# Kernel optimization log

Hardware: AMD Instinct MI355X
Metric: run time of the kernel (lower is better)

Reference implementation:

```python
import jax, jax.numpy as jnp
import numpy as np

H = 16        # num_attention_heads
KVH = 4       # num_key_value_heads
D = 128       # head_dim
K = 5         # query multiplier k
HID = 2048    # hidden_size = H * D
THETA = 10000.0


def rotate_half(x):
    h = x.shape[-1] // 2
    return jnp.concatenate([-x[..., h:], x[..., :h]], axis=-1)


def setup_inputs() -> dict:
    key = jax.random.key(0)
    ks = jax.random.split(key, 6)
    B, S = 1, 1024
    q_len = S - 1
    hidden_states = jax.random.normal(ks[0], (B, S, HID), jnp.float32)
    prev_hidden_states = jax.random.normal(ks[1], (B, S - 1, HID), jnp.float32)
    causal = jnp.tril(jnp.ones((q_len, q_len), bool))
    attention_mask = jnp.where(causal, 0.0, -1e9).astype(jnp.float32)[None, None]  # (1,1,q,kv)
    position_ids = jnp.arange(q_len, dtype=jnp.int64)[None]  # (1, kv_len)
    Wq = jax.random.normal(ks[2], (HID, H * D * K), jnp.float32) * 0.02
    Wkv = jax.random.normal(ks[3], (2 * HID, 2 * KVH * D), jnp.float32) * 0.02
    Wo = jax.random.normal(ks[4], (HID, HID), jnp.float32) * 0.02
    return {
        'hidden_states': hidden_states,
        'prev_hidden_states': prev_hidden_states,
        'attention_mask': attention_mask,
        'position_ids': position_ids,
        'Wq': Wq,
        'Wkv': Wkv,
        'Wo': Wo,
    }


def reference(hidden_states, prev_hidden_states, attention_mask, position_ids, Wq, Wkv, Wo):
    B = hidden_states.shape[0]  # must be 1 for this module's broadcasting
    # feature-dim concat of previous layer states with shifted current states
    prev = jnp.concatenate([prev_hidden_states, hidden_states[:, :-1]], axis=-1)  # (B, S-1, 2*HID)
    hs = hidden_states[:, 1:]  # training-mode slice -> (B, q_len, HID)
    q_len = hs.shape[1]
    kv_len = prev.shape[1]

    q = hs @ Wq                       # (B, q_len, H*D*K)
    kv = prev @ Wkv                   # (B, kv_len, 2*KVH*D)
    k_st, v_st = jnp.split(kv, 2, axis=-1)

    # faithful raw reshape: (B, q_len, H*D*K) -> (B*K, q_len, H, D) -> (B*K, H, q_len, D)
    q = q.reshape(B * K, -1, H, D).transpose(0, 2, 1, 3)
    k_st = k_st.reshape(B, kv_len, KVH, D).transpose(0, 2, 1, 3)   # (B, KVH, kv, D)
    v_st = v_st.reshape(B, kv_len, KVH, D).transpose(0, 2, 1, 3)

    # RoPE (LlamaRotaryEmbedding)
    inv_freq = 1.0 / (THETA ** (jnp.arange(0, D, 2, dtype=jnp.float32) / D))  # (D/2,)
    freqs = position_ids.astype(jnp.float32)[..., None] * inv_freq            # (B, kv, D/2)
    emb = jnp.concatenate([freqs, freqs], axis=-1)                            # (B, kv, D)
    cos = jnp.cos(emb)[:, None]  # (B, 1, kv, D)
    sin = jnp.sin(emb)[:, None]
    q = q * cos[..., -q_len:, :] + rotate_half(q) * sin[..., -q_len:, :]
    k_st = k_st * cos[..., :kv_len, :] + rotate_half(k_st) * sin[..., :kv_len, :]

    # repeat_kv: (B, KVH, kv, D) -> (B, H, kv, D)
    n_rep = H // KVH
    k_rep = jnp.repeat(k_st, n_rep, axis=1)
    v_rep = jnp.repeat(v_st, n_rep, axis=1)

    # (B*K, H, q, D) @ (B, H, D, kv) -> broadcast over k variants (B==1)
    attn = jnp.matmul(q, jnp.swapaxes(k_rep, -1, -2)) / jnp.sqrt(jnp.float32(D))
    attn = attn + attention_mask
    attn = jax.nn.softmax(attn.astype(jnp.float32), axis=-1).astype(q.dtype)
    out = jnp.matmul(attn, v_rep)                 # (B*K, H, q, D)
    out = out.transpose(0, 2, 1, 3).reshape(B * K, q_len, HID)
    return out @ Wo                                # (B*K, q_len, HID)
```

## Files before the change

kernel.cpp:

```cpp
#include <hip/hip_runtime.h>
#include <cstddef>
#include <cstdint>

#define SQ    1023
#define HIDC  2048
#define NQC   10240
#define NKVC  1024

typedef unsigned short ushort_t;
typedef __bf16 bf16x8 __attribute__((ext_vector_type(8)));
typedef float  f32x4  __attribute__((ext_vector_type(4)));

__device__ __forceinline__ ushort_t f2bf(float x) {
  union { float f; uint32_t u; } v; v.f = x;
  uint32_t r = v.u + 0x7fffu + ((v.u >> 16) & 1u);
  return (ushort_t)(r >> 16);
}

__device__ __forceinline__ ushort_t f2bf_fast(float x) {
  __bf16 b = (__bf16)x;
  return __builtin_bit_cast(ushort_t, b);
}

__global__ void k_tables(float* __restrict__ cosT, float* __restrict__ sinT) {
  int idx = blockIdx.x * blockDim.x + threadIdx.x;
  if (idx >= SQ * 64) return;
  int t = idx >> 6, i = idx & 63;
  float inv = powf(10000.0f, -(float)i * (1.0f / 64.0f));
  float f = (float)t * inv;
  cosT[idx] = cosf(f);
  sinT[idx] = sinf(f);
}

__global__ void k_rope_q(const float* __restrict__ q, ushort_t* __restrict__ qb,
                         const float* __restrict__ cosT, const float* __restrict__ sinT) {
  int idx = blockIdx.x * blockDim.x + threadIdx.x;
  if (idx >= 5115 * 16 * 64) return;
  int d  = idx & 63;
  int h  = (idx >> 6) & 15;
  int st = idx >> 10;
  int t  = st % 1023;
  size_t base = (((size_t)st * 16) + h) * 128 + d;
  float x0 = q[base], x1 = q[base + 64];
  float c = cosT[t * 64 + d], s = sinT[t * 64 + d];
  const float sc = 0.1275174485f;
  qb[base]      = f2bf((x0 * c - x1 * s) * sc);
  qb[base + 64] = f2bf((x1 * c + x0 * s) * sc);
}

__global__ void k_rope_k(const float* __restrict__ kvp, ushort_t* __restrict__ kb,
                         const float* __restrict__ cosT, const float* __restrict__ sinT) {
  int idx = blockIdx.x * blockDim.x + threadIdx.x;
  if (idx >= SQ * 4 * 64) return;
  int d   = idx & 63;
  int kvh = (idx >> 6) & 3;
  int t   = idx >> 8;
  size_t src = (size_t)t * 1024 + kvh * 128 + d;
  float x0 = 0.f, x1 = 0.f;
  #pragma unroll
  for (int z = 0; z < 4; ++z) {
    x0 += kvp[(size_t)z * (SQ * 1024) + src];
    x1 += kvp[(size_t)z * (SQ * 1024) + src + 64];
  }
  float c = cosT[t * 64 + d], s = sinT[t * 64 + d];
  size_t dst = (size_t)t * 512 + kvh * 128 + d;
  kb[dst]      = f2bf(x0 * c - x1 * s);
  kb[dst + 64] = f2bf(x1 * c + x0 * s);
}

__global__ __launch_bounds__(256)
void k_vtrans(const float* __restrict__ kvp, ushort_t* __restrict__ vt) {
  __shared__ float tile[32][33];
  int v0 = blockIdx.x * 32;
  int t0 = blockIdx.y * 32;
  int r = threadIdx.x >> 5, c = threadIdx.x & 31;
  #pragma unroll
  for (int p = 0; p < 4; ++p) {
    int t = t0 + p * 8 + r;
    float s = 0.f;
    if (t < SQ) {
      size_t src = (size_t)t * 1024 + 512 + v0 + c;
      #pragma unroll
      for (int z = 0; z < 4; ++z) s += kvp[(size_t)z * (SQ * 1024) + src];
    }
    tile[p * 8 + r][c] = s;
  }
  __syncthreads();
  #pragma unroll
  for (int p = 0; p < 4; ++p) {
    int v = v0 + p * 8 + r;
    vt[(size_t)v * 1024 + t0 + c] = f2bf(tile[c][p * 8 + r]);
  }
}

__global__ void k_f2b(const float* __restrict__ in, ushort_t* __restrict__ out, int n) {
  int i = (blockIdx.x * blockDim.x + threadIdx.x) * 4;
  if (i >= n) return;
  float4 v = *reinterpret_cast<const float4*>(in + i);
  uint2 pk;
  pk.x = (uint32_t)f2bf(v.x) | ((uint32_t)f2bf(v.y) << 16);
  pk.y = (uint32_t)f2bf(v.z) | ((uint32_t)f2bf(v.w) << 16);
  *reinterpret_cast<uint2*>(out + i) = pk;
}

__global__ void k_concat_b(const float* __restrict__ prevh, const float* __restrict__ hidden,
                           ushort_t* __restrict__ out) {
  int i = (blockIdx.x * blockDim.x + threadIdx.x) * 4;
  if (i >= SQ * 4096) return;
  int r = i >> 12, c = i & 4095;
  const float* src = (c < 2048) ? (prevh + (size_t)r * 2048 + c)
                                : (hidden + (size_t)r * 2048 + (c - 2048));
  float4 v = *reinterpret_cast<const float4*>(src);
  uint2 pk;
  pk.x = (uint32_t)f2bf(v.x) | ((uint32_t)f2bf(v.y) << 16);
  pk.y = (uint32_t)f2bf(v.z) | ((uint32_t)f2bf(v.w) << 16);
  *reinterpret_cast<uint2*>(out + (size_t)r * 4096 + c) = pk;
}

__global__ __launch_bounds__(256)
void k_tconv(const float* __restrict__ in, ushort_t* __restrict__ out, int K, int N) {
  __shared__ float t[32][33];
  int n0 = blockIdx.x * 32, k0 = blockIdx.y * 32;
  int r = threadIdx.x >> 5, c = threadIdx.x & 31;
  #pragma unroll
  for (int p = 0; p < 4; ++p)
    t[p * 8 + r][c] = in[(size_t)(k0 + p * 8 + r) * N + n0 + c];
  __syncthreads();
  #pragma unroll
  for (int p = 0; p < 4; ++p)
    out[(size_t)(n0 + p * 8 + r) * K + k0 + c] = f2bf(t[c][p * 8 + r]);
}

__global__ __launch_bounds__(256)
void k_gemm3buf(const ushort_t* __restrict__ A, const ushort_t* __restrict__ Bt,
                float* __restrict__ C, int M, int N, int Kd)
{
  __shared__ __align__(16) ushort_t As[3][128 * 32];
  __shared__ __align__(16) ushort_t Bs[3][128 * 32];

  const int tid  = threadIdx.x;
  const int lane = tid & 63;
  const int w    = tid >> 6;
  const int wm   = w >> 1, wn = w & 1;
  const int fr   = lane & 15;
  const int kg   = (lane >> 4) * 8;
  const int m0   = blockIdx.y * 128, n0 = blockIdx.x * 128;

  const int lrow = lane >> 2;
  const int lk   = (lane & 3) * 8;

  f32x4 acc[4][4];
  #pragma unroll
  for (int i = 0; i < 4; ++i)
    #pragma unroll
    for (int j = 0; j < 4; ++j) acc[i][j] = (f32x4){0.f, 0.f, 0.f, 0.f};

  auto STAGE = [&](int b, int k0) {
    #pragma unroll
    for (int c = 0; c < 2; ++c) {
      int ch  = w + c * 4;
      int row = ch * 16 + lrow;
      const ushort_t* ga = A  + (size_t)(m0 + row) * Kd + k0 + lk;
      const ushort_t* gb = Bt + (size_t)(n0 + row) * Kd + k0 + lk;
      __builtin_amdgcn_global_load_lds(
          (const __attribute__((address_space(1))) void*)ga,
          (__attribute__((address_space(3))) void*)(&As[b][0] + ch * 512), 16, 0, 0);
      __builtin_amdgcn_global_load_lds(
          (const __attribute__((address_space(1))) void*)gb,
          (__attribute__((address_space(3))) void*)(&Bs[b][0] + ch * 512), 16, 0, 0);
    }
  };

  const int nt = Kd / 32;
  STAGE(0, 0);
  STAGE(1, 32);

  int cur = 0;
  for (int t = 0; t < nt; ++t) {
    if (t + 1 < nt) {
      asm volatile("s_waitcnt vmcnt(4)" ::: "memory");
    } else {
      asm volatile("s_waitcnt vmcnt(0)" ::: "memory");
    }
    __builtin_amdgcn_s_barrier();
    if (t + 2 < nt) {
      int sb = cur + 2; if (sb >= 3) sb -= 3;
      STAGE(sb, (t + 2) * 32);
    }

    bf16x8 av[4], bv[4];
    #pragma unroll
    for (int mi = 0; mi < 4; ++mi)
      av[mi] = *reinterpret_cast<const bf16x8*>(&As[cur][0] + (wm * 64 + mi * 16 + fr) * 32 + kg);
    #pragma unroll
    for (int nj = 0; nj < 4; ++nj)
      bv[nj] = *reinterpret_cast<const bf16x8*>(&Bs[cur][0] + (wn * 64 + nj * 16 + fr) * 32 + kg);
    #pragma unroll
    for (int mi = 0; mi < 4; ++mi)
      #pragma unroll
      for (int nj = 0; nj < 4; ++nj)
        acc[mi][nj] = __builtin_amdgcn_mfma_f32_16x16x32_bf16(av[mi], bv[nj], acc[mi][nj], 0, 0, 0);

    cur = (cur == 2) ? 0 : cur + 1;
  }

  #pragma unroll
  for (int mi = 0; mi < 4; ++mi) {
    #pragma unroll
    for (int nj = 0; nj < 4; ++nj) {
      int rbase = m0 + wm * 64 + mi * 16 + (lane >> 4) * 4;
      int col   = n0 + wn * 64 + nj * 16 + fr;
      #pragma unroll
      for (int r = 0; r < 4; ++r) {
        int gr = rbase + r;
        if (gr < M) C[(size_t)gr * N + col] = acc[mi][nj][r];
      }
    }
  }
}

__global__ __launch_bounds__(256)
void k_gemm64(const ushort_t* __restrict__ A, const ushort_t* __restrict__ Bt,
              float* __restrict__ C, int M, int N, int Kd, int kLen)
{
  __shared__ __align__(16) ushort_t As[64 * 32];
  __shared__ __align__(16) ushort_t Bs[128 * 32];

  const int tid  = threadIdx.x;
  const int lane = tid & 63;
  const int w    = tid >> 6;
  const int wm   = w >> 1, wn = w & 1;
  const int fr   = lane & 15;
  const int kg   = (lane >> 4) * 8;
  const int g4   = lane >> 4;
  const int l15  = lane & 15;
  const int m0   = blockIdx.y * 64, n0 = blockIdx.x * 128;
  const int kOff = blockIdx.z * kLen;
  C += (size_t)blockIdx.z * M * N;

  const int arow = tid >> 2, aslot = (tid & 3) * 8;

  f32x4 acc[2][4];
  #pragma unroll
  for (int i = 0; i < 2; ++i)
    #pragma unroll
    for (int j = 0; j < 4; ++j) acc[i][j] = (f32x4){0.f, 0.f, 0.f, 0.f};

  for (int k0 = kOff; k0 < kOff + kLen; k0 += 32) {
    {
      const ushort_t* ga = A + (size_t)(m0 + arow) * Kd + k0 + aslot;
      __builtin_amdgcn_global_load_lds(
          (const __attribute__((address_space(1))) void*)ga,
          (__attribute__((address_space(3))) void*)(As + w * 512), 16, 0, 0);
    }
    #pragma unroll
    for (int c = 0; c < 2; ++c) {
      int u = c * 256 + tid;
      const ushort_t* gb = Bt + (size_t)(n0 + (u >> 2)) * Kd + k0 + (u & 3) * 8;
      __builtin_amdgcn_global_load_lds(
          (const __attribute__((address_space(1))) void*)gb,
          (__attribute__((address_space(3))) void*)(Bs + (c * 256 + w * 64) * 8), 16, 0, 0);
    }
    __syncthreads();

    bf16x8 av[2], bv[4];
    #pragma unroll
    for (int mi = 0; mi < 2; ++mi)
      av[mi] = *reinterpret_cast<const bf16x8*>(As + (wm * 32 + mi * 16 + fr) * 32 + kg);
    #pragma unroll
    for (int nj = 0; nj < 4; ++nj)
      bv[nj] = *reinterpret_cast<const bf16x8*>(Bs + (wn * 64 + nj * 16 + fr) * 32 + kg);
    #pragma unroll
    for (int mi = 0; mi < 2; ++mi)
      #pragma unroll
      for (int nj = 0; nj < 4; ++nj)
        acc[mi][nj] = __builtin_amdgcn_mfma_f32_16x16x32_bf16(av[mi], bv[nj], acc[mi][nj], 0, 0, 0);
    __syncthreads();
  }

  #pragma unroll
  for (int mi = 0; mi < 2; ++mi) {
    #pragma unroll
    for (int nj = 0; nj < 4; ++nj) {
      int rbase = m0 + wm * 32 + mi * 16 + g4 * 4;
      int col   = n0 + wn * 64 + nj * 16 + l15;
      #pragma unroll
      for (int r = 0; r < 4; ++r) {
        int gr = rbase + r;
        if (gr < M) C[(size_t)gr * N + col] = acc[mi][nj][r];
      }
    }
  }
}

__global__ __launch_bounds__(256)
void k_attn_mfma(const ushort_t* __restrict__ qb, const ushort_t* __restrict__ kb,
                 const ushort_t* __restrict__ vt, ushort_t* __restrict__ oattb)
{
  __shared__ __align__(16) ushort_t Ks[64 * 128];
  __shared__ __align__(16) ushort_t Vs[128 * 64];
  __shared__ __align__(16) ushort_t Ps[4][16 * 64];

  const int tid  = threadIdx.x;
  const int lane = tid & 63;
  const int w    = tid >> 6;
  const int l15  = lane & 15;
  const int g4   = lane >> 4;
  const int gh   = blockIdx.x;
  const int g = gh >> 4, h = gh & 15, kvh = (gh & 15) >> 2;
  const int qt = 15 - blockIdx.y;
  const int t0 = qt * 64;

  bf16x8 av[4];
  {
    int t = t0 + w * 16 + l15;
    const ushort_t* qrow = qb + (((size_t)(g * SQ + t)) * 16 + h) * 128;
    #pragma unroll
    for (int kk = 0; kk < 4; ++kk)
      av[kk] = *reinterpret_cast<const bf16x8*>(qrow + kk * 32 + g4 * 8);
  }

  f32x4 acc[8];
  #pragma unroll
  for (int dt = 0; dt < 8; ++dt) acc[dt] = (f32x4){0.f, 0.f, 0.f, 0.f};
  float m[4], l[4];
  #pragma unroll
  for (int r = 0; r < 4; ++r) { m[r] = -1e30f; l[r] = 0.f; }

  ushort_t* pw = &Ps[w][0];

  for (int jt = 0; jt <= qt; ++jt) {
    int u0 = jt * 64;
    #pragma unroll
    for (int i = 0; i < 4; ++i) {
      int c = (w * 4 + i) * 64 + lane;
      int kv = c >> 4, sl = c & 15;
      const ushort_t* srck = kb + (size_t)(u0 + kv) * 512 + kvh * 128 + ((sl ^ (kv & 7)) << 3);
      __builtin_amdgcn_global_load_lds(
          (const __attribute__((address_space(1))) void*)srck,
          (__attribute__((address_space(3))) void*)(Ks + (w * 4 + i) * 512), 16, 0, 0);
      int d = c >> 3, sv = c & 7;
      const ushort_t* srcv = vt + (size_t)(kvh * 128 + d) * 1024 + u0 + ((sv ^ (d & 7)) << 3);
      __builtin_amdgcn_global_load_lds(
          (const __attribute__((address_space(1))) void*)srcv,
          (__attribute__((address_space(3))) void*)(Vs + (w * 4 + i) * 512), 16, 0, 0);
    }
    __syncthreads();

    f32x4 S[4];
    #pragma unroll
    for (int ct = 0; ct < 4; ++ct) S[ct] = (f32x4){0.f, 0.f, 0.f, 0.f};
    #pragma unroll
    for (int ct = 0; ct < 4; ++ct) {
      int kv = ct * 16 + l15;
      #pragma unroll
      for (int kk = 0; kk < 4; ++kk) {
        bf16x8 bv = *reinterpret_cast<const bf16x8*>(
            Ks + kv * 128 + ((((kk << 2) | g4) ^ (kv & 7)) << 3));
        S[ct] = __builtin_amdgcn_mfma_f32_16x16x32_bf16(av[kk], bv, S[ct], 0, 0, 0);
      }
    }
    if (jt == qt) {
      #pragma unroll
      for (int ct = 0; ct < 4; ++ct) {
        int u = u0 + ct * 16 + l15;
        #pragma unroll
        for (int r = 0; r < 4; ++r) {
          int t = t0 + w * 16 + g4 * 4 + r;
          if (u > t) S[ct][r] = -1e30f;
        }
      }
    }
    float tm[4];
    #pragma unroll
    for (int r = 0; r < 4; ++r) {
      float t1 = fmaxf(fmaxf(S[0][r], S[1][r]), fmaxf(S[2][r], S[3][r]));
      t1 = fmaxf(t1, __shfl_xor(t1, 1));
      t1 = fmaxf(t1, __shfl_xor(t1, 2));
      t1 = fmaxf(t1, __shfl_xor(t1, 4));
      t1 = fmaxf(t1, __shfl_xor(t1, 8));
      tm[r] = t1;
    }
    bool need = (tm[0] > m[0] + 8.f) || (tm[1] > m[1] + 8.f) ||
                (tm[2] > m[2] + 8.f) || (tm[3] > m[3] + 8.f);
    if (__any(need)) {
      #pragma unroll
      for (int r = 0; r < 4; ++r) {
        float mn = fmaxf(m[r], tm[r]);
        float corr = exp2f(m[r] - mn);
        m[r] = mn;
        l[r] *= corr;
        #pragma unroll
        for (int dt = 0; dt < 8; ++dt) acc[dt][r] *= corr;
      }
    }
    #pragma unroll
    for (int r = 0; r < 4; ++r) {
      float ps = 0.f;
      #pragma unroll
      for (int ct = 0; ct < 4; ++ct) {
        float p = exp2f(S[ct][r] - m[r]);
        S[ct][r] = p;
        ps += p;
      }
      ps += __shfl_xor(ps, 1);
      ps += __shfl_xor(ps, 2);
      ps += __shfl_xor(ps, 4);
      ps += __shfl_xor(ps, 8);
      l[r] += ps;
    }

    #pragma unroll
    for (int ct = 0; ct < 4; ++ct) {
      int kv = ct * 16 + l15;
      #pragma unroll
      for (int r = 0; r < 4; ++r) {
        int q = g4 * 4 + r;
        pw[q * 64 + ((((kv >> 3) ^ (q & 7)) << 3) | (kv & 7))] = f2bf_fast(S[ct][r]);
      }
    }
    #pragma unroll
    for (int kk = 0; kk < 2; ++kk) {
      bf16x8 pa = *reinterpret_cast<const bf16x8*>(
          pw + l15 * 64 + ((((kk << 2) | g4) ^ (l15 & 7)) << 3));
      #pragma unroll
      for (int dt = 0; dt < 8; ++dt) {
        int d = dt * 16 + l15;
        bf16x8 vv = *reinterpret_cast<const bf16x8*>(
            Vs + d * 64 + ((((kk << 2) | g4) ^ (d & 7)) << 3));
        acc[dt] = __builtin_amdgcn_mfma_f32_16x16x32_bf16(pa, vv, acc[dt], 0, 0, 0);
      }
    }
    __syncthreads();
  }

  #pragma unroll
  for (int r = 0; r < 4; ++r) {
    int t = t0 + w * 16 + g4 * 4 + r;
    if (t >= SQ) continue;
    float inv = 1.f / l[r];
    ushort_t* dst = oattb + ((size_t)(g * SQ + t)) * 2048 + h * 128;
    #pragma unroll
    for (int dt = 0; dt < 8; ++dt)
      dst[dt * 16 + l15] = f2bf_fast(acc[dt][r] * inv);
  }
}

extern "C" void kernel_launch(void* const* d_in, const int* in_sizes, int n_in,
                              void* d_out, int out_size, void* d_ws, size_t ws_size,
                              hipStream_t stream) {
  const float* hidden = (const float*)d_in[0];
  const float* prevh  = (const float*)d_in[1];
  const float* Wq     = (const float*)d_in[4];
  const float* Wkv    = (const float*)d_in[5];
  const float* Wo     = (const float*)d_in[6];
  float* out = (float*)d_out;

  char* ws = (char*)d_ws;
  float*    kvp   = (float*)ws;                        ws += (size_t)4 * SQ * 1024 * 4;
  float*    cosT  = (float*)ws;                        ws += (size_t)65472 * 4;
  float*    sinT  = (float*)ws;                        ws += (size_t)65472 * 4;
  ushort_t* qbb   = (ushort_t*)ws;                     ws += (size_t)5120 * 2048 * 2;
  ushort_t* kb    = (ushort_t*)ws;                     ws += (size_t)1024 * 512 * 2;
  ushort_t* vtb   = (ushort_t*)ws;                     ws += (size_t)512 * 1024 * 2;
  ushort_t* hbf   = (ushort_t*)ws;                     ws += (size_t)1024 * 2048 * 2;
  ushort_t* akv   = (ushort_t*)ws;                     ws += (size_t)1024 * 4096 * 2;
  ushort_t* oattb = (ushort_t*)ws;                     ws += (size_t)5120 * 2048 * 2;
  ushort_t* wqt   = (ushort_t*)ws;                     ws += (size_t)10240 * 2048 * 2;
  ushort_t* wkvt  = (ushort_t*)ws;                     ws += (size_t)1024 * 4096 * 2;
  ushort_t* wot   = (ushort_t*)ws;                     ws += (size_t)2048 * 2048 * 2;

  float* qp = out;

  k_tables<<<dim3((SQ * 64 + 255) / 256), dim3(256), 0, stream>>>(cosT, sinT);

  k_tconv<<<dim3(NQC / 32, HIDC / 32), dim3(256), 0, stream>>>(Wq, wqt, HIDC, NQC);
  k_tconv<<<dim3(NKVC / 32, 4096 / 32), dim3(256), 0, stream>>>(Wkv, wkvt, 4096, NKVC);
  k_tconv<<<dim3(HIDC / 32, HIDC / 32), dim3(256), 0, stream>>>(Wo, wot, HIDC, HIDC);

  k_f2b<<<dim3((SQ * 2048 / 4 + 255) / 256), dim3(256), 0, stream>>>(hidden + 2048, hbf, SQ * 2048);
  k_concat_b<<<dim3((SQ * 4096 / 4 + 255) / 256), dim3(256), 0, stream>>>(prevh, hidden, akv);

  k_gemm3buf<<<dim3(NQC / 128, 8), dim3(256), 0, stream>>>(hbf, wqt, qp, SQ, NQC, 2048);
  k_gemm64<<<dim3(NKVC / 128, 16, 4), dim3(256), 0, stream>>>(akv, wkvt, kvp, SQ, NKVC, 4096, 1024);

  k_rope_q<<<dim3((5115 * 16 * 64 + 255) / 256), dim3(256), 0, stream>>>(qp, qbb, cosT, sinT);
  k_rope_k<<<dim3((SQ * 4 * 64 + 255) / 256), dim3(256), 0, stream>>>(kvp, kb, cosT, sinT);
  k_vtrans<<<dim3(16, 32), dim3(256), 0, stream>>>(kvp, vtb);

  k_attn_mfma<<<dim3(80, 16), dim3(256), 0, stream>>>(qbb, kb, vtb, oattb);

  k_gemm3buf<<<dim3(HIDC / 128, 40), dim3(256), 0, stream>>>(oattb, wot, out, 5115, HIDC, 2048);
}
```

Measured before the change: 286.5 us.

## Fuse Q RoPE into Q projection GEMM epilogue and use raw v_exp

A dedicated Q-projection GEMM now applies RoPE and the softmax scale in its epilogue and writes bf16 Q directly. This drops the fp32 Q intermediate (about 42 MB written and read back) and the separate rope kernel launch. The n-tile column layout is arranged so that each thread holds both d and d+64 halves. Separately, exp2f in the attention softmax is replaced by a raw v_exp_f32 inline asm, which skips denormal and range handling.

```diff
diff --git a/kernel.cpp b/kernel.cpp
--- a/kernel.cpp
+++ b/kernel.cpp
@@ -20,6 +20,12 @@
 __device__ __forceinline__ ushort_t f2bf_fast(float x) {
   __bf16 b = (__bf16)x;
   return __builtin_bit_cast(ushort_t, b);
+}
+
+__device__ __forceinline__ float fexp2(float x) {
+  float r;
+  asm("v_exp_f32 %0, %1\n\ts_nop 0" : "=v"(r) : "v"(x));
+  return r;
 }
 
 __global__ void k_tables(float* __restrict__ cosT, float* __restrict__ sinT) {
@@ -30,22 +36,6 @@
   float f = (float)t * inv;
   cosT[idx] = cosf(f);
   sinT[idx] = sinf(f);
-}
-
-__global__ void k_rope_q(const float* __restrict__ q, ushort_t* __restrict__ qb,
-                         const float* __restrict__ cosT, const float* __restrict__ sinT) {
-  int idx = blockIdx.x * blockDim.x + threadIdx.x;
-  if (idx >= 5115 * 16 * 64) return;
-  int d  = idx & 63;
-  int h  = (idx >> 6) & 15;
-  int st = idx >> 10;
-  int t  = st % 1023;
-  size_t base = (((size_t)st * 16) + h) * 128 + d;
-  float x0 = q[base], x1 = q[base + 64];
-  float c = cosT[t * 64 + d], s = sinT[t * 64 + d];
-  const float sc = 0.1275174485f;
-  qb[base]      = f2bf((x0 * c - x1 * s) * sc);
-  qb[base + 64] = f2bf((x1 * c + x0 * s) * sc);
 }
 
 __global__ void k_rope_k(const float* __restrict__ kvp, ushort_t* __restrict__ kb,
@@ -132,6 +122,110 @@
 }
 
 __global__ __launch_bounds__(256)
+void k_gemm_rope(const ushort_t* __restrict__ A, const ushort_t* __restrict__ Bt,
+                 ushort_t* __restrict__ Q, const float* __restrict__ cosT,
+                 const float* __restrict__ sinT)
+{
+  const int Kd = 2048, N = NQC;
+  __shared__ __align__(16) ushort_t As[3][128 * 32];
+  __shared__ __align__(16) ushort_t Bs[3][128 * 32];
+
+  const int tid  = threadIdx.x;
+  const int lane = tid & 63;
+  const int w    = tid >> 6;
+  const int wm   = w >> 1, wn = w & 1;
+  const int fr   = lane & 15;
+  const int kg   = (lane >> 4) * 8;
+  const int g4   = lane >> 4;
+  const int m0   = blockIdx.y * 128, n0 = blockIdx.x * 128;
+
+  const int lrow = lane >> 2;
+  const int lk   = (lane & 3) * 8;
+
+  f32x4 acc[4][4];
+  #pragma unroll
+  for (int i = 0; i < 4; ++i)
+    #pragma unroll
+    for (int j = 0; j < 4; ++j) acc[i][j] = (f32x4){0.f, 0.f, 0.f, 0.f};
+
+  auto STAGE = [&](int b, int k0) {
+    #pragma unroll
+    for (int c = 0; c < 2; ++c) {
+      int ch  = w + c * 4;
+      int row = ch * 16 + lrow;
+      const ushort_t* ga = A  + (size_t)(m0 + row) * Kd + k0 + lk;
+      const ushort_t* gb = Bt + (size_t)(n0 + row) * Kd + k0 + lk;
+      __builtin_amdgcn_global_load_lds(
+          (const __attribute__((address_space(1))) void*)ga,
+          (__attribute__((address_space(3))) void*)(&As[b][0] + ch * 512), 16, 0, 0);
+      __builtin_amdgcn_global_load_lds(
+          (const __attribute__((address_space(1))) void*)gb,
+          (__attribute__((address_space(3))) void*)(&Bs[b][0] + ch * 512), 16, 0, 0);
+    }
+  };
+
+  const int nt = Kd / 32;
+  STAGE(0, 0);
+  STAGE(1, 32);
+
+  int cur = 0;
+  for (int t = 0; t < nt; ++t) {
+    if (t + 1 < nt) {
+      asm volatile("s_waitcnt vmcnt(4)" ::: "memory");
+    } else {
+      asm volatile("s_waitcnt vmcnt(0)" ::: "memory");
+    }
+    __builtin_amdgcn_s_barrier();
+    if (t + 2 < nt) {
+      int sb = cur + 2; if (sb >= 3) sb -= 3;
+      STAGE(sb, (t + 2) * 32);
+    }
+
+    bf16x8 av[4], bv[4];
+    #pragma unroll
+    for (int mi = 0; mi < 4; ++mi)
+      av[mi] = *reinterpret_cast<const bf16x8*>(&As[cur][0] + (wm * 64 + mi * 16 + fr) * 32 + kg);
+    #pragma unroll
+    for (int nj = 0; nj < 4; ++nj) {
+      int colOff = wn * 32 + (nj & 1) * 16 + (nj >> 1) * 64;
+      bv[nj] = *reinterpret_cast<const bf16x8*>(&Bs[cur][0] + (colOff + fr) * 32 + kg);
+    }
+    #pragma unroll
+    for (int mi = 0; mi < 4; ++mi)
+      #pragma unroll
+      for (int nj = 0; nj < 4; ++nj)
+        acc[mi][nj] = __builtin_amdgcn_mfma_f32_16x16x32_bf16(av[mi], bv[nj], acc[mi][nj], 0, 0, 0);
+
+    cur = (cur == 2) ? 0 : cur + 1;
+  }
+
+  const float sc = 0.1275174485f;
+  const int nChunk = n0 >> 11;
+  #pragma unroll
+  for (int mi = 0; mi < 4; ++mi) {
+    #pragma unroll
+    for (int r = 0; r < 4; ++r) {
+      int gr = m0 + wm * 64 + mi * 16 + g4 * 4 + r;
+      if (gr >= SQ) continue;
+      int st  = gr * 5 + nChunk;
+      int tau = st % 1023;
+      const float* ct = cosT + tau * 64;
+      const float* stb = sinT + tau * 64;
+      #pragma unroll
+      for (int njp = 0; njp < 2; ++njp) {
+        int dd = wn * 32 + njp * 16 + fr;
+        float c = ct[dd], s = stb[dd];
+        float x0 = acc[mi][njp][r];
+        float x1 = acc[mi][njp + 2][r];
+        size_t base = (size_t)gr * 10240 + n0 + dd;
+        Q[base]      = f2bf_fast((x0 * c - x1 * s) * sc);
+        Q[base + 64] = f2bf_fast((x1 * c + x0 * s) * sc);
+      }
+    }
+  }
+}
+
+__global__ __launch_bounds__(256)
 void k_gemm3buf(const ushort_t* __restrict__ A, const ushort_t* __restrict__ Bt,
                 float* __restrict__ C, int M, int N, int Kd)
 {
@@ -387,7 +481,7 @@
       #pragma unroll
       for (int r = 0; r < 4; ++r) {
         float mn = fmaxf(m[r], tm[r]);
-        float corr = exp2f(m[r] - mn);
+        float corr = fexp2(m[r] - mn);
         m[r] = mn;
         l[r] *= corr;
         #pragma unroll
@@ -399,7 +493,7 @@
       float ps = 0.f;
       #pragma unroll
       for (int ct = 0; ct < 4; ++ct) {
-        float p = exp2f(S[ct][r] - m[r]);
+        float p = fexp2(S[ct][r] - m[r]);
         S[ct][r] = p;
         ps += p;
       }
@@ -470,8 +564,6 @@
   ushort_t* wkvt  = (ushort_t*)ws;                     ws += (size_t)1024 * 4096 * 2;
   ushort_t* wot   = (ushort_t*)ws;                     ws += (size_t)2048 * 2048 * 2;
 
-  float* qp = out;
-
   k_tables<<<dim3((SQ * 64 + 255) / 256), dim3(256), 0, stream>>>(cosT, sinT);
 
   k_tconv<<<dim3(NQC / 32, HIDC / 32), dim3(256), 0, stream>>>(Wq, wqt, HIDC, NQC);
@@ -481,10 +573,9 @@
   k_f2b<<<dim3((SQ * 2048 / 4 + 255) / 256), dim3(256), 0, stream>>>(hidden + 2048, hbf, SQ * 2048);
   k_concat_b<<<dim3((SQ * 4096 / 4 + 255) / 256), dim3(256), 0, stream>>>(prevh, hidden, akv);
 
-  k_gemm3buf<<<dim3(NQC / 128, 8), dim3(256), 0, stream>>>(hbf, wqt, qp, SQ, NQC, 2048);
+  k_gemm_rope<<<dim3(NQC / 128, 8), dim3(256), 0, stream>>>(hbf, wqt, qbb, cosT, sinT);
   k_gemm64<<<dim3(NKVC / 128, 16, 4), dim3(256), 0, stream>>>(akv, wkvt, kvp, SQ, NKVC, 4096, 1024);
 
-  k_rope_q<<<dim3((5115 * 16 * 64 + 255) / 256), dim3(256), 0, stream>>>(qp, qbb, cosT, sinT);
   k_rope_k<<<dim3((SQ * 4 * 64 + 255) / 256), dim3(256), 0, stream>>>(kvp, kb, cosT, sinT);
   k_vtrans<<<dim3(16, 32), dim3(256), 0, stream>>>(kvp, vtb);
 
```

Result: faster. 279.8 us (-2.3%).
